# Kernel optimization log

Measured on AMD Instinct MI355X. Metric: run time of the kernel, lower is better.

## Reference

```python
import jax, jax.numpy as jnp
import numpy as np

D_MODEL = 64  # per-head dim used in the scale sqrt(d_model*2)
B, H, S, D = 4, 16, 2048, 64


def setup_inputs() -> dict:
    key = jax.random.key(0)
    kq, kk, kv, kd, ke, km = jax.random.split(key, 6)
    return {
        "Q": jax.random.normal(kq, (B, H, S, D), dtype=jnp.float32),
        "K": jax.random.normal(kk, (B, H, S, D), dtype=jnp.float32),
        "V": jax.random.normal(kv, (B, H, S, D), dtype=jnp.float32),
        "distance_matrix": jax.random.uniform(kd, (B, S, S), dtype=jnp.float32),
        "energy_matrix": jax.random.uniform(ke, (B, S, S), dtype=jnp.float32),
        "mask": jax.random.randint(km, (B, 1, S, S), 0, 2, dtype=jnp.int32),
    }


def reference(Q, K, V, distance_matrix, energy_matrix, mask):
    # distance_matrix and energy_matrix are unused by the original forward.
    scale = 1.0 / np.sqrt(D_MODEL * 2).astype(np.float32)
    scores = jnp.einsum("bhqd,bhkd->bhqk", Q, K) * scale  # [B,H,S,S]
    scores = jnp.where(mask == 0, jnp.float32(-1e9), scores)
    attn = jax.nn.softmax(scores, axis=-1)
    context = jnp.einsum("bhqk,bhkd->bhqd", attn, V)  # [B,H,S,D]
    return context
```

## Files before the change

### kernel.cpp

```cpp
#include <hip/hip_runtime.h>
#include <stdint.h>

#define DEVINL __device__ __forceinline__

typedef float f32x4 __attribute__((ext_vector_type(4)));
typedef float f32x2 __attribute__((ext_vector_type(2)));
typedef short s16x8 __attribute__((ext_vector_type(8)));
typedef short s16x4 __attribute__((ext_vector_type(4)));
typedef unsigned int u32x4 __attribute__((ext_vector_type(4)));

constexpr int Bb = 4, Hh = 16, Ss = 2048, Dd = 64;
constexpr float SCALE = 0.088388347648318447f;
constexpr float QSC = 0.088388347648318447f * 1.4426950408889634f;

DEVINL short f2bf(float x) {
  union { float f; unsigned u; } c; c.f = x;
  unsigned r = (c.u + 0x7fffu + ((c.u >> 16) & 1u)) >> 16;
  return (short)r;
}

DEVINL unsigned pkbf(float a, float b) {
  unsigned r;
  asm("v_cvt_pk_bf16_f32 %0, %1, %2" : "=v"(r) : "v"(a), "v"(b));
  return r;
}

DEVINL void gload_lds16(const short* g, short* l) {
  __builtin_amdgcn_global_load_lds(
      (const __attribute__((address_space(1))) void*)g,
      (__attribute__((address_space(3))) void*)l, 16, 0, 0);
}

__global__ void mask_to_bits(const int* __restrict__ mask,
                             unsigned long long* __restrict__ bits, int n) {
  int gid = blockIdx.x * blockDim.x + threadIdx.x;
  int stride = gridDim.x * blockDim.x;
  for (int i = gid; i < n; i += stride) {
    unsigned long long bal = __ballot(mask[i] != 0);
    if ((i & 63) == 0) bits[i >> 6] = bal;
  }
}

__global__ void kvconv(const float* __restrict__ K, const float* __restrict__ V,
                       short* __restrict__ Kimg, short* __restrict__ Vimg) {
  const int x = blockIdx.x;
  const int sel = x & 1;
  const int t = (x >> 1) & 31;
  const int bh = x >> 6;
  const int tid = threadIdx.x;
  if (sel == 0) {
    const float* Kp = K + ((size_t)bh * Ss + t * 64) * Dd;
    short* img = Kimg + ((size_t)bh * 32 + t) * 4096;
#pragma unroll
    for (int it = 0; it < 4; ++it) {
      int idx = tid + it * 256;
      int kv = idx >> 4, c = idx & 15;
      const float* kr = Kp + (size_t)kv * Dd;
      s16x4 sv;
      sv[0] = f2bf(kr[c]);
      sv[1] = f2bf(kr[c + 16]);
      sv[2] = f2bf(kr[c + 32]);
      sv[3] = f2bf(kr[c + 48]);
      *(s16x4*)(img + kv * 64 + ((4 * c) ^ ((kv & 7) << 3))) = sv;
    }
  } else {
    const float* Vp = V + ((size_t)bh * Ss + t * 64) * Dd;
    short* img = Vimg + ((size_t)bh * 32 + t) * 4096;
    const int d = tid & 63, c4 = tid >> 6;
#pragma unroll
    for (int it = 0; it < 4; ++it) {
      int c = c4 * 4 + it;
      s16x4 sv;
      sv[0] = f2bf(Vp[(size_t)(c) * Dd + d]);
      sv[1] = f2bf(Vp[(size_t)(c + 16) * Dd + d]);
      sv[2] = f2bf(Vp[(size_t)(c + 32) * Dd + d]);
      sv[3] = f2bf(Vp[(size_t)(c + 48) * Dd + d]);
      *(s16x4*)(img + d * 64 + ((4 * c) ^ ((d & 7) << 3))) = sv;
    }
  }
}

__launch_bounds__(256, 4)
__global__ void attn2(const float* __restrict__ Q,
                      const unsigned long long* __restrict__ mbits,
                      const short* __restrict__ Kimg,
                      const short* __restrict__ Vimg,
                      float* __restrict__ Out) {
  __shared__ short lds[16384];

  const int tid = threadIdx.x;
  const int lane = tid & 63;
  const int w = tid >> 6;
  const int l15 = lane & 15;
  const int lq = lane >> 4;

  const int bid = blockIdx.x;
  const int h = bid & 15;
  const int qt = (bid >> 4) & 15;
  const int b = bid >> 8;
  const int bh = b * Hh + h;

  const float* Qp = Q + (size_t)bh * Ss * Dd;
  float* Op = Out + (size_t)bh * Ss * Dd;
  const short* Kt = Kimg + (size_t)bh * 32 * 4096;
  const short* Vt = Vimg + (size_t)bh * 32 * 4096;
  const int qbW = qt * 128 + w * 32;

  s16x8 qf[2][2];
#pragma unroll
  for (int qs = 0; qs < 2; ++qs) {
    const float* qrow = Qp + (size_t)(qbW + qs * 16 + l15) * Dd;
#pragma unroll
    for (int dh = 0; dh < 2; ++dh) {
      s16x8 f;
#pragma unroll
      for (int g = 0; g < 4; ++g) {
        f32x2 v = *(const f32x2*)(qrow + 16 * g + 4 * lq + 2 * dh);
        f[g] = f2bf(v[0] * QSC);
        f[g + 4] = f2bf(v[1] * QSC);
      }
      qf[qs][dh] = f;
    }
  }

  s16x8 onesA;
  {
    short o = (l15 == 0) ? (short)0x3F80 : (short)0;
#pragma unroll
    for (int j = 0; j < 8; ++j) onesA[j] = o;
  }

  f32x4 oacc[2][4];
  f32x4 lacc[2];
#pragma unroll
  for (int qs = 0; qs < 2; ++qs) {
    lacc[qs] = f32x4{0.f, 0.f, 0.f, 0.f};
#pragma unroll
    for (int ds = 0; ds < 4; ++ds) oacc[qs][ds] = f32x4{0.f, 0.f, 0.f, 0.f};
  }

  int off[4][2];
#pragma unroll
  for (int sub = 0; sub < 4; ++sub) {
    int row = sub * 16 + l15;
    int sw = (row & 7) << 3;
    off[sub][0] = row * 64 + ((16 * lq) ^ sw);
    off[sub][1] = row * 64 + ((16 * lq + 8) ^ sw);
  }

  const unsigned long long* mbq[2];
#pragma unroll
  for (int qs = 0; qs < 2; ++qs)
    mbq[qs] = mbits + (size_t)(b * Ss + qbW + qs * 16 + l15) * 32;

  auto stage = [&](int buf, int t) {
    short* Lb = lds + buf * 8192;
    const short* gk = Kt + t * 4096 + w * 512 + lane * 8;
    const short* gv = Vt + t * 4096 + w * 512 + lane * 8;
    gload_lds16(gk, Lb + w * 512);
    gload_lds16(gk + 2048, Lb + 2048 + w * 512);
    gload_lds16(gv, Lb + 4096 + w * 512);
    gload_lds16(gv + 2048, Lb + 6144 + w * 512);
  };

  stage(0, 0);

  for (int t = 0; t < 32; ++t) {
    const int cur = t & 1;
    unsigned long long mw0 = mbq[0][t];
    unsigned long long mw1 = mbq[1][t];
    __syncthreads();
    if (t < 31) stage(cur ^ 1, t + 1);

    const short* kb = lds + cur * 8192;
    const short* vb = kb + 4096;

    f32x4 bias[2][4];
#pragma unroll
    for (int qs = 0; qs < 2; ++qs) {
      const unsigned long long mw = qs ? mw1 : mw0;
      const unsigned mlo = ~(unsigned)(mw >> (4 * lq));
      const unsigned mhi = ~(unsigned)(mw >> (32 + 4 * lq));
#pragma unroll
      for (int sub = 0; sub < 4; ++sub) {
        const unsigned wsrc = (sub < 2) ? mlo : mhi;
        const int base = 16 * (sub & 1);
#pragma unroll
        for (int r = 0; r < 4; ++r) {
          int sb = ((int)(wsrc << (31 - (base + r)))) >> 31;
          bias[qs][sub][r] = __uint_as_float((unsigned)sb & 0xCE6E6B28u);
        }
      }
    }

    f32x4 sc[2][4];
    __builtin_amdgcn_s_setprio(1);
#pragma unroll
    for (int sub = 0; sub < 4; ++sub) {
      s16x8 k0 = *(const s16x8*)(kb + off[sub][0]);
      s16x8 k1 = *(const s16x8*)(kb + off[sub][1]);
#pragma unroll
      for (int qs = 0; qs < 2; ++qs) {
        f32x4 a = bias[qs][sub];
        a = __builtin_amdgcn_mfma_f32_16x16x32_bf16(k0, qf[qs][0], a, 0, 0, 0);
        a = __builtin_amdgcn_mfma_f32_16x16x32_bf16(k1, qf[qs][1], a, 0, 0, 0);
        sc[qs][sub] = a;
      }
    }
    __builtin_amdgcn_s_setprio(0);

    s16x8 pf[2][2];
#pragma unroll
    for (int qs = 0; qs < 2; ++qs) {
#pragma unroll
      for (int sub = 0; sub < 4; ++sub) {
        f32x4 s = sc[qs][sub];
#pragma unroll
        for (int r = 0; r < 4; ++r) s[r] = __builtin_amdgcn_exp2f(s[r]);
        sc[qs][sub] = s;
      }
#pragma unroll
      for (int kvh = 0; kvh < 2; ++kvh) {
        u32x4 wv;
        wv[0] = pkbf(sc[qs][0][2 * kvh], sc[qs][1][2 * kvh]);
        wv[1] = pkbf(sc[qs][2][2 * kvh], sc[qs][3][2 * kvh]);
        wv[2] = pkbf(sc[qs][0][2 * kvh + 1], sc[qs][1][2 * kvh + 1]);
        wv[3] = pkbf(sc[qs][2][2 * kvh + 1], sc[qs][3][2 * kvh + 1]);
        pf[qs][kvh] = __builtin_bit_cast(s16x8, wv);
      }
    }

    __builtin_amdgcn_s_setprio(1);
#pragma unroll
    for (int ds = 0; ds < 4; ++ds) {
      s16x8 v0 = *(const s16x8*)(vb + off[ds][0]);
      s16x8 v1 = *(const s16x8*)(vb + off[ds][1]);
#pragma unroll
      for (int qs = 0; qs < 2; ++qs) {
        f32x4 a = oacc[qs][ds];
        a = __builtin_amdgcn_mfma_f32_16x16x32_bf16(v0, pf[qs][0], a, 0, 0, 0);
        a = __builtin_amdgcn_mfma_f32_16x16x32_bf16(v1, pf[qs][1], a, 0, 0, 0);
        oacc[qs][ds] = a;
      }
    }
#pragma unroll
    for (int qs = 0; qs < 2; ++qs) {
      lacc[qs] = __builtin_amdgcn_mfma_f32_16x16x32_bf16(onesA, pf[qs][0], lacc[qs], 0, 0, 0);
      lacc[qs] = __builtin_amdgcn_mfma_f32_16x16x32_bf16(onesA, pf[qs][1], lacc[qs], 0, 0, 0);
    }
    __builtin_amdgcn_s_setprio(0);
  }

#pragma unroll
  for (int qs = 0; qs < 2; ++qs) {
    float l = __shfl(lacc[qs][0], l15);
    float inv = 1.f / l;
    float* orow = Op + (size_t)(qbW + qs * 16 + l15) * Dd;
#pragma unroll
    for (int ds = 0; ds < 4; ++ds) {
      f32x4 v = oacc[qs][ds];
      v *= inv;
      *(f32x4*)(orow + ds * 16 + 4 * lq) = v;
    }
  }
}

template<bool USEBITS>
__launch_bounds__(256, 2)
__global__ void attn_fwd(const float* __restrict__ Q, const float* __restrict__ K,
                         const float* __restrict__ V, const int* __restrict__ mask,
                         const unsigned long long* __restrict__ mbits,
                         float* __restrict__ Out) {
  __shared__ short Ks[64 * 64];
  __shared__ short Vs[64 * 64];

  const int tid = threadIdx.x;
  const int lane = tid & 63;
  const int w = tid >> 6;
  const int l15 = lane & 15;
  const int lq = lane >> 4;

  const int bid = blockIdx.x;
  const int h = bid & 15;
  const int qt = (bid >> 4) & 7;
  const int b = bid >> 7;

  const int bh = b * Hh + h;
  const float* Qp = Q + (size_t)bh * Ss * Dd;
  const float* Kp = K + (size_t)bh * Ss * Dd;
  const float* Vp = V + (size_t)bh * Ss * Dd;
  float* Op = Out + (size_t)bh * Ss * Dd;

  const int qbW = qt * 256 + w * 64;

  s16x8 qf[4][2];
#pragma unroll
  for (int qs = 0; qs < 4; ++qs) {
    const float* qrow = Qp + (size_t)(qbW + qs * 16 + l15) * Dd;
#pragma unroll
    for (int dh = 0; dh < 2; ++dh) {
      s16x8 f;
#pragma unroll
      for (int g = 0; g < 4; ++g) {
        f32x2 v = *(const f32x2*)(qrow + 16 * g + 4 * lq + 2 * dh);
        f[g] = f2bf(v[0]);
        f[g + 4] = f2bf(v[1]);
      }
      qf[qs][dh] = f;
    }
  }

  f32x4 oacc[4][4];
  float mrun[4], lrun[4];
#pragma unroll
  for (int qs = 0; qs < 4; ++qs) {
    mrun[qs] = -1e30f;
    lrun[qs] = 0.f;
#pragma unroll
    for (int ds = 0; ds < 4; ++ds) oacc[qs][ds] = f32x4{0.f, 0.f, 0.f, 0.f};
  }

  for (int kv0 = 0; kv0 < Ss; kv0 += 64) {
    __syncthreads();
#pragma unroll
    for (int p = 0; p < 4; ++p) {
      int f = tid + p * 256;
      int kv = f >> 4;
      int c = f & 15;
      const float* krow = Kp + (size_t)(kv0 + kv) * Dd;
      s16x4 sv;
      sv[0] = f2bf(krow[c]);
      sv[1] = f2bf(krow[c + 16]);
      sv[2] = f2bf(krow[c + 32]);
      sv[3] = f2bf(krow[c + 48]);
      *(s16x4*)(Ks + kv * 64 + ((4 * c) ^ ((kv & 7) << 3))) = sv;
    }
#pragma unroll
    for (int p = 0; p < 4; ++p) {
      int f = tid + p * 256;
      int kv = f >> 4;
      int c = f & 15;
      f32x4 v = *(const f32x4*)(Vp + (size_t)(kv0 + kv) * Dd + 4 * c);
      int pv = (kv & 15) * 4 + (kv >> 4);
#pragma unroll
      for (int i = 0; i < 4; ++i) {
        int d = 4 * c + i;
        Vs[d * 64 + (pv ^ ((d & 7) << 3))] = f2bf(v[i]);
      }
    }
    __syncthreads();

    s16x8 kf[4][2];
#pragma unroll
    for (int sub = 0; sub < 4; ++sub) {
      int row = sub * 16 + l15;
      const short* base = Ks + row * 64;
      int sw = (row & 7) << 3;
      kf[sub][0] = *(const s16x8*)(base + ((16 * lq + 0) ^ sw));
      kf[sub][1] = *(const s16x8*)(base + ((16 * lq + 8) ^ sw));
    }
    s16x8 vf[4][2];
#pragma unroll
    for (int ds = 0; ds < 4; ++ds) {
      int row = ds * 16 + l15;
      const short* base = Vs + row * 64;
      int sw = (row & 7) << 3;
      vf[ds][0] = *(const s16x8*)(base + ((16 * lq + 0) ^ sw));
      vf[ds][1] = *(const s16x8*)(base + ((16 * lq + 8) ^ sw));
    }

    const int kvw = kv0 >> 6;
#pragma unroll
    for (int qs = 0; qs < 4; ++qs) {
      f32x4 sc[4];
#pragma unroll
      for (int sub = 0; sub < 4; ++sub) {
        f32x4 a = f32x4{0.f, 0.f, 0.f, 0.f};
        a = __builtin_amdgcn_mfma_f32_16x16x32_bf16(kf[sub][0], qf[qs][0], a, 0, 0, 0);
        a = __builtin_amdgcn_mfma_f32_16x16x32_bf16(kf[sub][1], qf[qs][1], a, 0, 0, 0);
        sc[sub] = a;
      }

      const int q = qbW + qs * 16 + l15;
      unsigned long long mw = 0;
      if constexpr (USEBITS) mw = mbits[(size_t)(b * Ss + q) * 32 + kvw];

      float tm = -3e38f;
#pragma unroll
      for (int sub = 0; sub < 4; ++sub) {
        f32x4 s = sc[sub];
        if constexpr (USEBITS) {
          unsigned nib = (unsigned)((mw >> (16 * sub + 4 * lq)) & 0xFULL);
#pragma unroll
          for (int r = 0; r < 4; ++r) {
            float sv = s[r] * SCALE;
            sv = ((nib >> r) & 1u) ? sv : -1e9f;
            s[r] = sv;
            tm = fmaxf(tm, sv);
          }
        } else {
          const int* mrow = mask + ((size_t)b * Ss + q) * Ss + kv0 + 16 * sub + 4 * lq;
          int4 mi = *(const int4*)mrow;
          int mv[4] = {mi.x, mi.y, mi.z, mi.w};
#pragma unroll
          for (int r = 0; r < 4; ++r) {
            float sv = s[r] * SCALE;
            sv = mv[r] ? sv : -1e9f;
            s[r] = sv;
            tm = fmaxf(tm, sv);
          }
        }
        sc[sub] = s;
      }
      tm = fmaxf(tm, __shfl_xor(tm, 16));
      tm = fmaxf(tm, __shfl_xor(tm, 32));
      float mnew = fmaxf(mrun[qs], tm);
      float corr = __expf(mrun[qs] - mnew);
      mrun[qs] = mnew;

      float ps = 0.f;
#pragma unroll
      for (int sub = 0; sub < 4; ++sub) {
        f32x4 s = sc[sub];
#pragma unroll
        for (int r = 0; r < 4; ++r) {
          float p = __expf(s[r] - mnew);
          s[r] = p;
          ps += p;
        }
        sc[sub] = s;
      }
      ps += __shfl_xor(ps, 16);
      ps += __shfl_xor(ps, 32);
      lrun[qs] = lrun[qs] * corr + ps;
#pragma unroll
      for (int ds = 0; ds < 4; ++ds) oacc[qs][ds] *= corr;

      s16x8 pf[2];
#pragma unroll
      for (int kvh = 0; kvh < 2; ++kvh) {
        s16x8 f;
#pragma unroll
        for (int j = 0; j < 8; ++j) f[j] = f2bf(sc[j & 3][2 * kvh + (j >> 2)]);
        pf[kvh] = f;
      }
#pragma unroll
      for (int ds = 0; ds < 4; ++ds) {
        f32x4 a = oacc[qs][ds];
        a = __builtin_amdgcn_mfma_f32_16x16x32_bf16(vf[ds][0], pf[0], a, 0, 0, 0);
        a = __builtin_amdgcn_mfma_f32_16x16x32_bf16(vf[ds][1], pf[1], a, 0, 0, 0);
        oacc[qs][ds] = a;
      }
    }
  }

#pragma unroll
  for (int qs = 0; qs < 4; ++qs) {
    float inv = 1.f / lrun[qs];
    float* orow = Op + (size_t)(qbW + qs * 16 + l15) * Dd;
#pragma unroll
    for (int ds = 0; ds < 4; ++ds) {
      f32x4 v = oacc[qs][ds];
      v *= inv;
      *(f32x4*)(orow + ds * 16 + 4 * lq) = v;
    }
  }
}

extern "C" void kernel_launch(void* const* d_in, const int* in_sizes, int n_in,
                              void* d_out, int out_size, void* d_ws, size_t ws_size,
                              hipStream_t stream) {
  const float* Q = (const float*)d_in[0];
  const float* K = (const float*)d_in[1];
  const float* V = (const float*)d_in[2];
  const int* mask = (const int*)d_in[5];
  float* out = (float*)d_out;

  const int nmask = Bb * Ss * Ss;
  const size_t bitsB = (size_t)(nmask / 64) * 8;
  const size_t imgB = (size_t)Bb * Hh * 32 * 4096 * 2;
  const size_t need = bitsB + 2 * imgB;

  if (d_ws && ws_size >= need) {
    unsigned long long* bits = (unsigned long long*)d_ws;
    short* Kimg = (short*)((char*)d_ws + bitsB);
    short* Vimg = (short*)((char*)d_ws + bitsB + imgB);
    mask_to_bits<<<2048, 256, 0, stream>>>(mask, bits, nmask);
    kvconv<<<Bb * Hh * 32 * 2, 256, 0, stream>>>(K, V, Kimg, Vimg);
    attn2<<<Bb * Hh * (Ss / 128), 256, 0, stream>>>(Q, bits, Kimg, Vimg, out);
  } else if (d_ws && ws_size >= bitsB) {
    unsigned long long* bits = (unsigned long long*)d_ws;
    mask_to_bits<<<2048, 256, 0, stream>>>(mask, bits, nmask);
    attn_fwd<true><<<Bb * Hh * (Ss / 256), 256, 0, stream>>>(Q, K, V, mask, bits, out);
  } else {
    attn_fwd<false><<<Bb * Hh * (Ss / 256), 256, 0, stream>>>(Q, K, V, mask, nullptr, out);
  }
}
```

Baseline: 134.4 us.

## Halve per-wave query tile, double grid, and remap blocks for XCD locality

Each wave now handles 16 query rows instead of 32, so a block covers 64 queries and the grid doubles to 2048 blocks. Launch bounds rise to 5 blocks per SM to exploit the lower register use. Block indices are remapped with an 8-way interleave so blocks sharing the same batch-head land on the same XCD, improving L2 reuse of the K/V images. The trade-off is that each K/V tile loaded into LDS is reused by half as many query rows, doubling K/V staging traffic and the number of barriers per unit of work.

```diff
diff --git a/kernel.cpp b/kernel.cpp
--- a/kernel.cpp
+++ b/kernel.cpp
@@ -80,7 +80,7 @@
   }
 }
 
-__launch_bounds__(256, 4)
+__launch_bounds__(256, 5)
 __global__ void attn2(const float* __restrict__ Q,
                       const unsigned long long* __restrict__ mbits,
                       const short* __restrict__ Kimg,
@@ -94,22 +94,20 @@
   const int l15 = lane & 15;
   const int lq = lane >> 4;
 
-  const int bid = blockIdx.x;
-  const int h = bid & 15;
-  const int qt = (bid >> 4) & 15;
-  const int b = bid >> 8;
-  const int bh = b * Hh + h;
+  const int nb = ((blockIdx.x & 7) << 8) | (blockIdx.x >> 3);
+  const int qt = nb & 31;
+  const int bh = nb >> 5;
+  const int b = bh >> 4;
 
   const float* Qp = Q + (size_t)bh * Ss * Dd;
   float* Op = Out + (size_t)bh * Ss * Dd;
   const short* Kt = Kimg + (size_t)bh * 32 * 4096;
   const short* Vt = Vimg + (size_t)bh * 32 * 4096;
-  const int qbW = qt * 128 + w * 32;
-
-  s16x8 qf[2][2];
-#pragma unroll
-  for (int qs = 0; qs < 2; ++qs) {
-    const float* qrow = Qp + (size_t)(qbW + qs * 16 + l15) * Dd;
+  const int qbW = qt * 64 + w * 16;
+
+  s16x8 qf[2];
+  {
+    const float* qrow = Qp + (size_t)(qbW + l15) * Dd;
 #pragma unroll
     for (int dh = 0; dh < 2; ++dh) {
       s16x8 f;
@@ -119,7 +117,7 @@
         f[g] = f2bf(v[0] * QSC);
         f[g + 4] = f2bf(v[1] * QSC);
       }
-      qf[qs][dh] = f;
+      qf[dh] = f;
     }
   }
 
@@ -130,14 +128,10 @@
     for (int j = 0; j < 8; ++j) onesA[j] = o;
   }
 
-  f32x4 oacc[2][4];
-  f32x4 lacc[2];
-#pragma unroll
-  for (int qs = 0; qs < 2; ++qs) {
-    lacc[qs] = f32x4{0.f, 0.f, 0.f, 0.f};
-#pragma unroll
-    for (int ds = 0; ds < 4; ++ds) oacc[qs][ds] = f32x4{0.f, 0.f, 0.f, 0.f};
-  }
+  f32x4 oacc[4];
+  f32x4 lacc = f32x4{0.f, 0.f, 0.f, 0.f};
+#pragma unroll
+  for (int ds = 0; ds < 4; ++ds) oacc[ds] = f32x4{0.f, 0.f, 0.f, 0.f};
 
   int off[4][2];
 #pragma unroll
@@ -148,10 +142,7 @@
     off[sub][1] = row * 64 + ((16 * lq + 8) ^ sw);
   }
 
-  const unsigned long long* mbq[2];
-#pragma unroll
-  for (int qs = 0; qs < 2; ++qs)
-    mbq[qs] = mbits + (size_t)(b * Ss + qbW + qs * 16 + l15) * 32;
+  const unsigned long long* mbq = mbits + (size_t)(b * Ss + qbW + l15) * 32;
 
   auto stage = [&](int buf, int t) {
     short* Lb = lds + buf * 8192;
@@ -167,18 +158,15 @@
 
   for (int t = 0; t < 32; ++t) {
     const int cur = t & 1;
-    unsigned long long mw0 = mbq[0][t];
-    unsigned long long mw1 = mbq[1][t];
+    unsigned long long mw = mbq[t];
     __syncthreads();
     if (t < 31) stage(cur ^ 1, t + 1);
 
     const short* kb = lds + cur * 8192;
     const short* vb = kb + 4096;
 
-    f32x4 bias[2][4];
-#pragma unroll
-    for (int qs = 0; qs < 2; ++qs) {
-      const unsigned long long mw = qs ? mw1 : mw0;
+    f32x4 bias[4];
+    {
       const unsigned mlo = ~(unsigned)(mw >> (4 * lq));
       const unsigned mhi = ~(unsigned)(mw >> (32 + 4 * lq));
 #pragma unroll
@@ -188,46 +176,40 @@
 #pragma unroll
         for (int r = 0; r < 4; ++r) {
           int sb = ((int)(wsrc << (31 - (base + r)))) >> 31;
-          bias[qs][sub][r] = __uint_as_float((unsigned)sb & 0xCE6E6B28u);
+          bias[sub][r] = __uint_as_float((unsigned)sb & 0xCE6E6B28u);
         }
       }
     }
 
-    f32x4 sc[2][4];
+    f32x4 sc[4];
     __builtin_amdgcn_s_setprio(1);
 #pragma unroll
     for (int sub = 0; sub < 4; ++sub) {
       s16x8 k0 = *(const s16x8*)(kb + off[sub][0]);
       s16x8 k1 = *(const s16x8*)(kb + off[sub][1]);
-#pragma unroll
-      for (int qs = 0; qs < 2; ++qs) {
-        f32x4 a = bias[qs][sub];
-        a = __builtin_amdgcn_mfma_f32_16x16x32_bf16(k0, qf[qs][0], a, 0, 0, 0);
-        a = __builtin_amdgcn_mfma_f32_16x16x32_bf16(k1, qf[qs][1], a, 0, 0, 0);
-        sc[qs][sub] = a;
-      }
+      f32x4 a = bias[sub];
+      a = __builtin_amdgcn_mfma_f32_16x16x32_bf16(k0, qf[0], a, 0, 0, 0);
+      a = __builtin_amdgcn_mfma_f32_16x16x32_bf16(k1, qf[1], a, 0, 0, 0);
+      sc[sub] = a;
     }
     __builtin_amdgcn_s_setprio(0);
 
-    s16x8 pf[2][2];
-#pragma unroll
-    for (int qs = 0; qs < 2; ++qs) {
-#pragma unroll
-      for (int sub = 0; sub < 4; ++sub) {
-        f32x4 s = sc[qs][sub];
-#pragma unroll
-        for (int r = 0; r < 4; ++r) s[r] = __builtin_amdgcn_exp2f(s[r]);
-        sc[qs][sub] = s;
-      }
-#pragma unroll
-      for (int kvh = 0; kvh < 2; ++kvh) {
-        u32x4 wv;
-        wv[0] = pkbf(sc[qs][0][2 * kvh], sc[qs][1][2 * kvh]);
-        wv[1] = pkbf(sc[qs][2][2 * kvh], sc[qs][3][2 * kvh]);
-        wv[2] = pkbf(sc[qs][0][2 * kvh + 1], sc[qs][1][2 * kvh + 1]);
-        wv[3] = pkbf(sc[qs][2][2 * kvh + 1], sc[qs][3][2 * kvh + 1]);
-        pf[qs][kvh] = __builtin_bit_cast(s16x8, wv);
-      }
+    s16x8 pf[2];
+#pragma unroll
+    for (int sub = 0; sub < 4; ++sub) {
+      f32x4 s = sc[sub];
+#pragma unroll
+      for (int r = 0; r < 4; ++r) s[r] = __builtin_amdgcn_exp2f(s[r]);
+      sc[sub] = s;
+    }
+#pragma unroll
+    for (int kvh = 0; kvh < 2; ++kvh) {
+      u32x4 wv;
+      wv[0] = pkbf(sc[0][2 * kvh], sc[1][2 * kvh]);
+      wv[1] = pkbf(sc[2][2 * kvh], sc[3][2 * kvh]);
+      wv[2] = pkbf(sc[0][2 * kvh + 1], sc[1][2 * kvh + 1]);
+      wv[3] = pkbf(sc[2][2 * kvh + 1], sc[3][2 * kvh + 1]);
+      pf[kvh] = __builtin_bit_cast(s16x8, wv);
     }
 
     __builtin_amdgcn_s_setprio(1);
@@ -235,30 +217,23 @@
     for (int ds = 0; ds < 4; ++ds) {
       s16x8 v0 = *(const s16x8*)(vb + off[ds][0]);
       s16x8 v1 = *(const s16x8*)(vb + off[ds][1]);
-#pragma unroll
-      for (int qs = 0; qs < 2; ++qs) {
-        f32x4 a = oacc[qs][ds];
-        a = __builtin_amdgcn_mfma_f32_16x16x32_bf16(v0, pf[qs][0], a, 0, 0, 0);
-        a = __builtin_amdgcn_mfma_f32_16x16x32_bf16(v1, pf[qs][1], a, 0, 0, 0);
-        oacc[qs][ds] = a;
-      }
-    }
-#pragma unroll
-    for (int qs = 0; qs < 2; ++qs) {
-      lacc[qs] = __builtin_amdgcn_mfma_f32_16x16x32_bf16(onesA, pf[qs][0], lacc[qs], 0, 0, 0);
-      lacc[qs] = __builtin_amdgcn_mfma_f32_16x16x32_bf16(onesA, pf[qs][1], lacc[qs], 0, 0, 0);
-    }
+      f32x4 a = oacc[ds];
+      a = __builtin_amdgcn_mfma_f32_16x16x32_bf16(v0, pf[0], a, 0, 0, 0);
+      a = __builtin_amdgcn_mfma_f32_16x16x32_bf16(v1, pf[1], a, 0, 0, 0);
+      oacc[ds] = a;
+    }
+    lacc = __builtin_amdgcn_mfma_f32_16x16x32_bf16(onesA, pf[0], lacc, 0, 0, 0);
+    lacc = __builtin_amdgcn_mfma_f32_16x16x32_bf16(onesA, pf[1], lacc, 0, 0, 0);
     __builtin_amdgcn_s_setprio(0);
   }
 
-#pragma unroll
-  for (int qs = 0; qs < 2; ++qs) {
-    float l = __shfl(lacc[qs][0], l15);
+  {
+    float l = __shfl(lacc[0], l15);
     float inv = 1.f / l;
-    float* orow = Op + (size_t)(qbW + qs * 16 + l15) * Dd;
+    float* orow = Op + (size_t)(qbW + l15) * Dd;
 #pragma unroll
     for (int ds = 0; ds < 4; ++ds) {
-      f32x4 v = oacc[qs][ds];
+      f32x4 v = oacc[ds];
       v *= inv;
       *(f32x4*)(orow + ds * 16 + 4 * lq) = v;
     }
@@ -487,7 +462,7 @@
     short* Vimg = (short*)((char*)d_ws + bitsB + imgB);
     mask_to_bits<<<2048, 256, 0, stream>>>(mask, bits, nmask);
     kvconv<<<Bb * Hh * 32 * 2, 256, 0, stream>>>(K, V, Kimg, Vimg);
-    attn2<<<Bb * Hh * (Ss / 128), 256, 0, stream>>>(Q, bits, Kimg, Vimg, out);
+    attn2<<<Bb * Hh * (Ss / 64), 256, 0, stream>>>(Q, bits, Kimg, Vimg, out);
   } else if (d_ws && ws_size >= bitsB) {
     unsigned long long* bits = (unsigned long long*)d_ws;
     mask_to_bits<<<2048, 256, 0, stream>>>(mask, bits, nmask);
```

Result: slower. 144.0 us (+7.1%).

## Fuse prep kernels and load K/V fragments directly to registers

Applied to the files above, without the earlier changes.

Merges the mask bit-packing and K/V bf16 conversion into one prep launch, and lays the K/V images out in MFMA fragment order so the attention kernel can load them straight from global memory into registers with no LDS or barriers. Each wave now handles 64 queries instead of 32 (256 per block, 512 blocks), and block indices are swizzled so that blocks sharing a head are grouped. K/V fragments for the next tile are prefetched into registers after each matmul phase. The intent is to remove LDS staging, barrier synchronisation and one launch. In exchange, register pressure and occupancy change, and loads go through L2 without explicit sharing between waves.

```diff
diff --git a/kernel.cpp b/kernel.cpp
--- a/kernel.cpp
+++ b/kernel.cpp
@@ -25,10 +25,212 @@
   return r;
 }
 
-DEVINL void gload_lds16(const short* g, short* l) {
-  __builtin_amdgcn_global_load_lds(
-      (const __attribute__((address_space(1))) void*)g,
-      (__attribute__((address_space(3))) void*)l, 16, 0, 0);
+__global__ void prep(const float* __restrict__ K, const float* __restrict__ V,
+                     const int* __restrict__ mask,
+                     short* __restrict__ Kimg, short* __restrict__ Vimg,
+                     unsigned long long* __restrict__ bits) {
+  const int x = blockIdx.x;
+  const int tid = threadIdx.x;
+  if (x < 4096) {
+    const int sel = x & 1;
+    const int t = (x >> 1) & 31;
+    const int bh = x >> 6;
+    short* img = (sel ? Vimg : Kimg) + ((size_t)bh * 32 + t) * 4096;
+    const float* src = (sel ? V : K) + (size_t)bh * Ss * Dd;
+#pragma unroll
+    for (int p = 0; p < 2; ++p) {
+      const int pr = tid + p * 256;
+      const int f = pr >> 6;
+      const int lane = pr & 63;
+      const int l15 = lane & 15, lq = lane >> 4;
+      const int P = 16 * lq + 8 * (f & 1);
+      const int fs = f >> 1;
+      s16x8 o;
+      if (sel == 0) {
+        const float* kr = src + (size_t)(t * 64 + fs * 16 + l15) * Dd + (P >> 2);
+#pragma unroll
+        for (int jj = 0; jj < 2; ++jj)
+#pragma unroll
+          for (int m = 0; m < 4; ++m)
+            o[jj * 4 + m] = f2bf(kr[jj + 16 * m]);
+      } else {
+        const float* vc = src + (size_t)(t * 64 + (P >> 2)) * Dd + fs * 16 + l15;
+#pragma unroll
+        for (int jj = 0; jj < 2; ++jj)
+#pragma unroll
+          for (int m = 0; m < 4; ++m)
+            o[jj * 4 + m] = f2bf(vc[(size_t)(jj + 16 * m) * Dd]);
+      }
+      *(s16x8*)(img + pr * 8) = o;
+    }
+  } else {
+    const int gid = (x - 4096) * 256 + tid;
+    const int stride = 1024 * 256;
+    const int n = Bb * Ss * Ss;
+    for (int i = gid; i < n; i += stride) {
+      unsigned long long bal = __ballot(mask[i] != 0);
+      if ((i & 63) == 0) bits[i >> 6] = bal;
+    }
+  }
+}
+
+__launch_bounds__(256, 2)
+__global__ void attn3(const float* __restrict__ Q,
+                      const unsigned long long* __restrict__ mbits,
+                      const short* __restrict__ Kimg,
+                      const short* __restrict__ Vimg,
+                      float* __restrict__ Out) {
+  const int tid = threadIdx.x;
+  const int lane = tid & 63;
+  const int w = tid >> 6;
+  const int l15 = lane & 15;
+  const int lq = lane >> 4;
+
+  const int nb = ((blockIdx.x & 7) << 6) | (blockIdx.x >> 3);
+  const int qt = nb & 7;
+  const int bh = nb >> 3;
+  const int b = bh >> 4;
+
+  const float* Qp = Q + (size_t)bh * Ss * Dd;
+  float* Op = Out + (size_t)bh * Ss * Dd;
+  const short* Kt = Kimg + (size_t)bh * 32 * 4096 + lane * 8;
+  const short* Vt = Vimg + (size_t)bh * 32 * 4096 + lane * 8;
+  const int qbW = qt * 256 + w * 64;
+
+  s16x8 qf[4][2];
+#pragma unroll
+  for (int qs = 0; qs < 4; ++qs) {
+    const float* qrow = Qp + (size_t)(qbW + qs * 16 + l15) * Dd;
+#pragma unroll
+    for (int dh = 0; dh < 2; ++dh) {
+      s16x8 f;
+#pragma unroll
+      for (int g = 0; g < 4; ++g) {
+        f32x2 v = *(const f32x2*)(qrow + 16 * g + 4 * lq + 2 * dh);
+        f[g] = f2bf(v[0] * QSC);
+        f[g + 4] = f2bf(v[1] * QSC);
+      }
+      qf[qs][dh] = f;
+    }
+  }
+
+  s16x8 onesA;
+  {
+    short o = (l15 == 0) ? (short)0x3F80 : (short)0;
+#pragma unroll
+    for (int j = 0; j < 8; ++j) onesA[j] = o;
+  }
+
+  f32x4 oacc[4][4];
+  f32x4 lacc[4];
+#pragma unroll
+  for (int qs = 0; qs < 4; ++qs) {
+    lacc[qs] = f32x4{0.f, 0.f, 0.f, 0.f};
+#pragma unroll
+    for (int ds = 0; ds < 4; ++ds) oacc[qs][ds] = f32x4{0.f, 0.f, 0.f, 0.f};
+  }
+
+  const unsigned long long* mbq = mbits + (size_t)(b * Ss + qbW + l15) * 32;
+
+  s16x8 kf[8], vf[8];
+#pragma unroll
+  for (int f = 0; f < 8; ++f) kf[f] = *(const s16x8*)(Kt + f * 512);
+#pragma unroll
+  for (int f = 0; f < 8; ++f) vf[f] = *(const s16x8*)(Vt + f * 512);
+
+  for (int t = 0; t < 32; ++t) {
+    unsigned long long mw[4];
+#pragma unroll
+    for (int qs = 0; qs < 4; ++qs) mw[qs] = mbq[qs * 512 + t];
+
+    f32x4 sc[4][4];
+#pragma unroll
+    for (int qs = 0; qs < 4; ++qs) {
+      const unsigned mlo = ~(unsigned)(mw[qs] >> (4 * lq));
+      const unsigned mhi = ~(unsigned)(mw[qs] >> (32 + 4 * lq));
+#pragma unroll
+      for (int sub = 0; sub < 4; ++sub) {
+        const unsigned wsrc = (sub < 2) ? mlo : mhi;
+        const int base = 16 * (sub & 1);
+#pragma unroll
+        for (int r = 0; r < 4; ++r) {
+          int sb = ((int)(wsrc << (31 - (base + r)))) >> 31;
+          sc[qs][sub][r] = __uint_as_float((unsigned)sb & 0xCE6E6B28u);
+        }
+      }
+    }
+
+    __builtin_amdgcn_s_setprio(1);
+#pragma unroll
+    for (int sub = 0; sub < 4; ++sub)
+#pragma unroll
+      for (int qs = 0; qs < 4; ++qs) {
+        sc[qs][sub] = __builtin_amdgcn_mfma_f32_16x16x32_bf16(kf[sub * 2], qf[qs][0], sc[qs][sub], 0, 0, 0);
+        sc[qs][sub] = __builtin_amdgcn_mfma_f32_16x16x32_bf16(kf[sub * 2 + 1], qf[qs][1], sc[qs][sub], 0, 0, 0);
+      }
+    __builtin_amdgcn_s_setprio(0);
+
+    if (t < 31) {
+      const short* nk = Kt + (t + 1) * 4096;
+#pragma unroll
+      for (int f = 0; f < 8; ++f) kf[f] = *(const s16x8*)(nk + f * 512);
+    }
+
+    s16x8 pf[4][2];
+#pragma unroll
+    for (int qs = 0; qs < 4; ++qs) {
+#pragma unroll
+      for (int sub = 0; sub < 4; ++sub) {
+        f32x4 s = sc[qs][sub];
+#pragma unroll
+        for (int r = 0; r < 4; ++r) s[r] = __builtin_amdgcn_exp2f(s[r]);
+        sc[qs][sub] = s;
+      }
+#pragma unroll
+      for (int kvh = 0; kvh < 2; ++kvh) {
+        u32x4 wv;
+        wv[0] = pkbf(sc[qs][0][2 * kvh], sc[qs][1][2 * kvh]);
+        wv[1] = pkbf(sc[qs][2][2 * kvh], sc[qs][3][2 * kvh]);
+        wv[2] = pkbf(sc[qs][0][2 * kvh + 1], sc[qs][1][2 * kvh + 1]);
+        wv[3] = pkbf(sc[qs][2][2 * kvh + 1], sc[qs][3][2 * kvh + 1]);
+        pf[qs][kvh] = __builtin_bit_cast(s16x8, wv);
+      }
+    }
+
+    __builtin_amdgcn_s_setprio(1);
+#pragma unroll
+    for (int ds = 0; ds < 4; ++ds)
+#pragma unroll
+      for (int qs = 0; qs < 4; ++qs) {
+        oacc[qs][ds] = __builtin_amdgcn_mfma_f32_16x16x32_bf16(vf[ds * 2], pf[qs][0], oacc[qs][ds], 0, 0, 0);
+        oacc[qs][ds] = __builtin_amdgcn_mfma_f32_16x16x32_bf16(vf[ds * 2 + 1], pf[qs][1], oacc[qs][ds], 0, 0, 0);
+      }
+#pragma unroll
+    for (int qs = 0; qs < 4; ++qs) {
+      lacc[qs] = __builtin_amdgcn_mfma_f32_16x16x32_bf16(onesA, pf[qs][0], lacc[qs], 0, 0, 0);
+      lacc[qs] = __builtin_amdgcn_mfma_f32_16x16x32_bf16(onesA, pf[qs][1], lacc[qs], 0, 0, 0);
+    }
+    __builtin_amdgcn_s_setprio(0);
+
+    if (t < 31) {
+      const short* nv = Vt + (t + 1) * 4096;
+#pragma unroll
+      for (int f = 0; f < 8; ++f) vf[f] = *(const s16x8*)(nv + f * 512);
+    }
+  }
+
+#pragma unroll
+  for (int qs = 0; qs < 4; ++qs) {
+    float l = __shfl(lacc[qs][0], l15);
+    float inv = 1.f / l;
+    float* orow = Op + (size_t)(qbW + qs * 16 + l15) * Dd;
+#pragma unroll
+    for (int ds = 0; ds < 4; ++ds) {
+      f32x4 v = oacc[qs][ds];
+      v *= inv;
+      *(f32x4*)(orow + ds * 16 + 4 * lq) = v;
+    }
+  }
 }
 
 __global__ void mask_to_bits(const int* __restrict__ mask,
@@ -38,230 +240,6 @@
   for (int i = gid; i < n; i += stride) {
     unsigned long long bal = __ballot(mask[i] != 0);
     if ((i & 63) == 0) bits[i >> 6] = bal;
-  }
-}
-
-__global__ void kvconv(const float* __restrict__ K, const float* __restrict__ V,
-                       short* __restrict__ Kimg, short* __restrict__ Vimg) {
-  const int x = blockIdx.x;
-  const int sel = x & 1;
-  const int t = (x >> 1) & 31;
-  const int bh = x >> 6;
-  const int tid = threadIdx.x;
-  if (sel == 0) {
-    const float* Kp = K + ((size_t)bh * Ss + t * 64) * Dd;
-    short* img = Kimg + ((size_t)bh * 32 + t) * 4096;
-#pragma unroll
-    for (int it = 0; it < 4; ++it) {
-      int idx = tid + it * 256;
-      int kv = idx >> 4, c = idx & 15;
-      const float* kr = Kp + (size_t)kv * Dd;
-      s16x4 sv;
-      sv[0] = f2bf(kr[c]);
-      sv[1] = f2bf(kr[c + 16]);
-      sv[2] = f2bf(kr[c + 32]);
-      sv[3] = f2bf(kr[c + 48]);
-      *(s16x4*)(img + kv * 64 + ((4 * c) ^ ((kv & 7) << 3))) = sv;
-    }
-  } else {
-    const float* Vp = V + ((size_t)bh * Ss + t * 64) * Dd;
-    short* img = Vimg + ((size_t)bh * 32 + t) * 4096;
-    const int d = tid & 63, c4 = tid >> 6;
-#pragma unroll
-    for (int it = 0; it < 4; ++it) {
-      int c = c4 * 4 + it;
-      s16x4 sv;
-      sv[0] = f2bf(Vp[(size_t)(c) * Dd + d]);
-      sv[1] = f2bf(Vp[(size_t)(c + 16) * Dd + d]);
-      sv[2] = f2bf(Vp[(size_t)(c + 32) * Dd + d]);
-      sv[3] = f2bf(Vp[(size_t)(c + 48) * Dd + d]);
-      *(s16x4*)(img + d * 64 + ((4 * c) ^ ((d & 7) << 3))) = sv;
-    }
-  }
-}
-
-__launch_bounds__(256, 4)
-__global__ void attn2(const float* __restrict__ Q,
-                      const unsigned long long* __restrict__ mbits,
-                      const short* __restrict__ Kimg,
-                      const short* __restrict__ Vimg,
-                      float* __restrict__ Out) {
-  __shared__ short lds[16384];
-
-  const int tid = threadIdx.x;
-  const int lane = tid & 63;
-  const int w = tid >> 6;
-  const int l15 = lane & 15;
-  const int lq = lane >> 4;
-
-  const int bid = blockIdx.x;
-  const int h = bid & 15;
-  const int qt = (bid >> 4) & 15;
-  const int b = bid >> 8;
-  const int bh = b * Hh + h;
-
-  const float* Qp = Q + (size_t)bh * Ss * Dd;
-  float* Op = Out + (size_t)bh * Ss * Dd;
-  const short* Kt = Kimg + (size_t)bh * 32 * 4096;
-  const short* Vt = Vimg + (size_t)bh * 32 * 4096;
-  const int qbW = qt * 128 + w * 32;
-
-  s16x8 qf[2][2];
-#pragma unroll
-  for (int qs = 0; qs < 2; ++qs) {
-    const float* qrow = Qp + (size_t)(qbW + qs * 16 + l15) * Dd;
-#pragma unroll
-    for (int dh = 0; dh < 2; ++dh) {
-      s16x8 f;
-#pragma unroll
-      for (int g = 0; g < 4; ++g) {
-        f32x2 v = *(const f32x2*)(qrow + 16 * g + 4 * lq + 2 * dh);
-        f[g] = f2bf(v[0] * QSC);
-        f[g + 4] = f2bf(v[1] * QSC);
-      }
-      qf[qs][dh] = f;
-    }
-  }
-
-  s16x8 onesA;
-  {
-    short o = (l15 == 0) ? (short)0x3F80 : (short)0;
-#pragma unroll
-    for (int j = 0; j < 8; ++j) onesA[j] = o;
-  }
-
-  f32x4 oacc[2][4];
-  f32x4 lacc[2];
-#pragma unroll
-  for (int qs = 0; qs < 2; ++qs) {
-    lacc[qs] = f32x4{0.f, 0.f, 0.f, 0.f};
-#pragma unroll
-    for (int ds = 0; ds < 4; ++ds) oacc[qs][ds] = f32x4{0.f, 0.f, 0.f, 0.f};
-  }
-
-  int off[4][2];
-#pragma unroll
-  for (int sub = 0; sub < 4; ++sub) {
-    int row = sub * 16 + l15;
-    int sw = (row & 7) << 3;
-    off[sub][0] = row * 64 + ((16 * lq) ^ sw);
-    off[sub][1] = row * 64 + ((16 * lq + 8) ^ sw);
-  }
-
-  const unsigned long long* mbq[2];
-#pragma unroll
-  for (int qs = 0; qs < 2; ++qs)
-    mbq[qs] = mbits + (size_t)(b * Ss + qbW + qs * 16 + l15) * 32;
-
-  auto stage = [&](int buf, int t) {
-    short* Lb = lds + buf * 8192;
-    const short* gk = Kt + t * 4096 + w * 512 + lane * 8;
-    const short* gv = Vt + t * 4096 + w * 512 + lane * 8;
-    gload_lds16(gk, Lb + w * 512);
-    gload_lds16(gk + 2048, Lb + 2048 + w * 512);
-    gload_lds16(gv, Lb + 4096 + w * 512);
-    gload_lds16(gv + 2048, Lb + 6144 + w * 512);
-  };
-
-  stage(0, 0);
-
-  for (int t = 0; t < 32; ++t) {
-    const int cur = t & 1;
-    unsigned long long mw0 = mbq[0][t];
-    unsigned long long mw1 = mbq[1][t];
-    __syncthreads();
-    if (t < 31) stage(cur ^ 1, t + 1);
-
-    const short* kb = lds + cur * 8192;
-    const short* vb = kb + 4096;
-
-    f32x4 bias[2][4];
-#pragma unroll
-    for (int qs = 0; qs < 2; ++qs) {
-      const unsigned long long mw = qs ? mw1 : mw0;
-      const unsigned mlo = ~(unsigned)(mw >> (4 * lq));
-      const unsigned mhi = ~(unsigned)(mw >> (32 + 4 * lq));
-#pragma unroll
-      for (int sub = 0; sub < 4; ++sub) {
-        const unsigned wsrc = (sub < 2) ? mlo : mhi;
-        const int base = 16 * (sub & 1);
-#pragma unroll
-        for (int r = 0; r < 4; ++r) {
-          int sb = ((int)(wsrc << (31 - (base + r)))) >> 31;
-          bias[qs][sub][r] = __uint_as_float((unsigned)sb & 0xCE6E6B28u);
-        }
-      }
-    }
-
-    f32x4 sc[2][4];
-    __builtin_amdgcn_s_setprio(1);
-#pragma unroll
-    for (int sub = 0; sub < 4; ++sub) {
-      s16x8 k0 = *(const s16x8*)(kb + off[sub][0]);
-      s16x8 k1 = *(const s16x8*)(kb + off[sub][1]);
-#pragma unroll
-      for (int qs = 0; qs < 2; ++qs) {
-        f32x4 a = bias[qs][sub];
-        a = __builtin_amdgcn_mfma_f32_16x16x32_bf16(k0, qf[qs][0], a, 0, 0, 0);
-        a = __builtin_amdgcn_mfma_f32_16x16x32_bf16(k1, qf[qs][1], a, 0, 0, 0);
-        sc[qs][sub] = a;
-      }
-    }
-    __builtin_amdgcn_s_setprio(0);
-
-    s16x8 pf[2][2];
-#pragma unroll
-    for (int qs = 0; qs < 2; ++qs) {
-#pragma unroll
-      for (int sub = 0; sub < 4; ++sub) {
-        f32x4 s = sc[qs][sub];
-#pragma unroll
-        for (int r = 0; r < 4; ++r) s[r] = __builtin_amdgcn_exp2f(s[r]);
-        sc[qs][sub] = s;
-      }
-#pragma unroll
-      for (int kvh = 0; kvh < 2; ++kvh) {
-        u32x4 wv;
-        wv[0] = pkbf(sc[qs][0][2 * kvh], sc[qs][1][2 * kvh]);
-        wv[1] = pkbf(sc[qs][2][2 * kvh], sc[qs][3][2 * kvh]);
-        wv[2] = pkbf(sc[qs][0][2 * kvh + 1], sc[qs][1][2 * kvh + 1]);
-        wv[3] = pkbf(sc[qs][2][2 * kvh + 1], sc[qs][3][2 * kvh + 1]);
-        pf[qs][kvh] = __builtin_bit_cast(s16x8, wv);
-      }
-    }
-
-    __builtin_amdgcn_s_setprio(1);
-#pragma unroll
-    for (int ds = 0; ds < 4; ++ds) {
-      s16x8 v0 = *(const s16x8*)(vb + off[ds][0]);
-      s16x8 v1 = *(const s16x8*)(vb + off[ds][1]);
-#pragma unroll
-      for (int qs = 0; qs < 2; ++qs) {
-        f32x4 a = oacc[qs][ds];
-        a = __builtin_amdgcn_mfma_f32_16x16x32_bf16(v0, pf[qs][0], a, 0, 0, 0);
-        a = __builtin_amdgcn_mfma_f32_16x16x32_bf16(v1, pf[qs][1], a, 0, 0, 0);
-        oacc[qs][ds] = a;
-      }
-    }
-#pragma unroll
-    for (int qs = 0; qs < 2; ++qs) {
-      lacc[qs] = __builtin_amdgcn_mfma_f32_16x16x32_bf16(onesA, pf[qs][0], lacc[qs], 0, 0, 0);
-      lacc[qs] = __builtin_amdgcn_mfma_f32_16x16x32_bf16(onesA, pf[qs][1], lacc[qs], 0, 0, 0);
-    }
-    __builtin_amdgcn_s_setprio(0);
-  }
-
-#pragma unroll
-  for (int qs = 0; qs < 2; ++qs) {
-    float l = __shfl(lacc[qs][0], l15);
-    float inv = 1.f / l;
-    float* orow = Op + (size_t)(qbW + qs * 16 + l15) * Dd;
-#pragma unroll
-    for (int ds = 0; ds < 4; ++ds) {
-      f32x4 v = oacc[qs][ds];
-      v *= inv;
-      *(f32x4*)(orow + ds * 16 + 4 * lq) = v;
-    }
   }
 }
 
@@ -485,9 +463,8 @@
     unsigned long long* bits = (unsigned long long*)d_ws;
     short* Kimg = (short*)((char*)d_ws + bitsB);
     short* Vimg = (short*)((char*)d_ws + bitsB + imgB);
-    mask_to_bits<<<2048, 256, 0, stream>>>(mask, bits, nmask);
-    kvconv<<<Bb * Hh * 32 * 2, 256, 0, stream>>>(K, V, Kimg, Vimg);
-    attn2<<<Bb * Hh * (Ss / 128), 256, 0, stream>>>(Q, bits, Kimg, Vimg, out);
+    prep<<<5120, 256, 0, stream>>>(K, V, mask, Kimg, Vimg, bits);
+    attn3<<<512, 256, 0, stream>>>(Q, bits, Kimg, Vimg, out);
   } else if (d_ws && ws_size >= bitsB) {
     unsigned long long* bits = (unsigned long long*)d_ws;
     mask_to_bits<<<2048, 256, 0, stream>>>(mask, bits, nmask);
```

After: 160.6 us. 19.5% more time.

## Merge mask packing and KV conversion into one kernel; interleave exp with MFMA

Applied to the files above, without the earlier changes.

Combines the mask-to-bitmask and K/V bf16 conversion kernels into a single prep launch, with blocks split by index. This removes one kernel launch and lets the two memory-bound jobs run at the same time. In the attention loop it splits the two query sub-tiles and interleaves the exp2 of one sub-tile with the MFMAs of the other, so transcendental work overlaps matrix-core work. This adds register pressure and depends on the compiler keeping the intended order.

```diff
diff --git a/kernel.cpp b/kernel.cpp
--- a/kernel.cpp
+++ b/kernel.cpp
@@ -31,51 +31,53 @@
       (__attribute__((address_space(3))) void*)l, 16, 0, 0);
 }
 
-__global__ void mask_to_bits(const int* __restrict__ mask,
-                             unsigned long long* __restrict__ bits, int n) {
-  int gid = blockIdx.x * blockDim.x + threadIdx.x;
-  int stride = gridDim.x * blockDim.x;
-  for (int i = gid; i < n; i += stride) {
-    unsigned long long bal = __ballot(mask[i] != 0);
-    if ((i & 63) == 0) bits[i >> 6] = bal;
-  }
-}
-
-__global__ void kvconv(const float* __restrict__ K, const float* __restrict__ V,
-                       short* __restrict__ Kimg, short* __restrict__ Vimg) {
+__global__ void prep(const float* __restrict__ K, const float* __restrict__ V,
+                     const int* __restrict__ mask,
+                     short* __restrict__ Kimg, short* __restrict__ Vimg,
+                     unsigned long long* __restrict__ bits) {
   const int x = blockIdx.x;
-  const int sel = x & 1;
-  const int t = (x >> 1) & 31;
-  const int bh = x >> 6;
   const int tid = threadIdx.x;
-  if (sel == 0) {
-    const float* Kp = K + ((size_t)bh * Ss + t * 64) * Dd;
-    short* img = Kimg + ((size_t)bh * 32 + t) * 4096;
-#pragma unroll
-    for (int it = 0; it < 4; ++it) {
-      int idx = tid + it * 256;
-      int kv = idx >> 4, c = idx & 15;
-      const float* kr = Kp + (size_t)kv * Dd;
-      s16x4 sv;
-      sv[0] = f2bf(kr[c]);
-      sv[1] = f2bf(kr[c + 16]);
-      sv[2] = f2bf(kr[c + 32]);
-      sv[3] = f2bf(kr[c + 48]);
-      *(s16x4*)(img + kv * 64 + ((4 * c) ^ ((kv & 7) << 3))) = sv;
+  if (x < 4096) {
+    const int sel = x & 1;
+    const int t = (x >> 1) & 31;
+    const int bh = x >> 6;
+    if (sel == 0) {
+      const float* Kp = K + ((size_t)bh * Ss + t * 64) * Dd;
+      short* img = Kimg + ((size_t)bh * 32 + t) * 4096;
+#pragma unroll
+      for (int it = 0; it < 4; ++it) {
+        int idx = tid + it * 256;
+        int kv = idx >> 4, c = idx & 15;
+        const float* kr = Kp + (size_t)kv * Dd;
+        s16x4 sv;
+        sv[0] = f2bf(kr[c]);
+        sv[1] = f2bf(kr[c + 16]);
+        sv[2] = f2bf(kr[c + 32]);
+        sv[3] = f2bf(kr[c + 48]);
+        *(s16x4*)(img + kv * 64 + ((4 * c) ^ ((kv & 7) << 3))) = sv;
+      }
+    } else {
+      const float* Vp = V + ((size_t)bh * Ss + t * 64) * Dd;
+      short* img = Vimg + ((size_t)bh * 32 + t) * 4096;
+      const int d = tid & 63, c4 = tid >> 6;
+#pragma unroll
+      for (int it = 0; it < 4; ++it) {
+        int c = c4 * 4 + it;
+        s16x4 sv;
+        sv[0] = f2bf(Vp[(size_t)(c) * Dd + d]);
+        sv[1] = f2bf(Vp[(size_t)(c + 16) * Dd + d]);
+        sv[2] = f2bf(Vp[(size_t)(c + 32) * Dd + d]);
+        sv[3] = f2bf(Vp[(size_t)(c + 48) * Dd + d]);
+        *(s16x4*)(img + d * 64 + ((4 * c) ^ ((d & 7) << 3))) = sv;
+      }
     }
   } else {
-    const float* Vp = V + ((size_t)bh * Ss + t * 64) * Dd;
-    short* img = Vimg + ((size_t)bh * 32 + t) * 4096;
-    const int d = tid & 63, c4 = tid >> 6;
-#pragma unroll
-    for (int it = 0; it < 4; ++it) {
-      int c = c4 * 4 + it;
-      s16x4 sv;
-      sv[0] = f2bf(Vp[(size_t)(c) * Dd + d]);
-      sv[1] = f2bf(Vp[(size_t)(c + 16) * Dd + d]);
-      sv[2] = f2bf(Vp[(size_t)(c + 32) * Dd + d]);
-      sv[3] = f2bf(Vp[(size_t)(c + 48) * Dd + d]);
-      *(s16x4*)(img + d * 64 + ((4 * c) ^ ((d & 7) << 3))) = sv;
+    const int gid = (x - 4096) * 256 + tid;
+    const int stride = 1024 * 256;
+    const int n = Bb * Ss * Ss;
+    for (int i = gid; i < n; i += stride) {
+      unsigned long long bal = __ballot(mask[i] != 0);
+      if ((i & 63) == 0) bits[i >> 6] = bal;
     }
   }
 }
@@ -175,79 +177,100 @@
     const short* kb = lds + cur * 8192;
     const short* vb = kb + 4096;
 
-    f32x4 bias[2][4];
-#pragma unroll
-    for (int qs = 0; qs < 2; ++qs) {
-      const unsigned long long mw = qs ? mw1 : mw0;
-      const unsigned mlo = ~(unsigned)(mw >> (4 * lq));
-      const unsigned mhi = ~(unsigned)(mw >> (32 + 4 * lq));
+    f32x4 bias0[4], bias1[4];
+    {
+      const unsigned mlo0 = ~(unsigned)(mw0 >> (4 * lq));
+      const unsigned mhi0 = ~(unsigned)(mw0 >> (32 + 4 * lq));
+      const unsigned mlo1 = ~(unsigned)(mw1 >> (4 * lq));
+      const unsigned mhi1 = ~(unsigned)(mw1 >> (32 + 4 * lq));
 #pragma unroll
       for (int sub = 0; sub < 4; ++sub) {
-        const unsigned wsrc = (sub < 2) ? mlo : mhi;
+        const unsigned w0 = (sub < 2) ? mlo0 : mhi0;
+        const unsigned w1 = (sub < 2) ? mlo1 : mhi1;
         const int base = 16 * (sub & 1);
 #pragma unroll
         for (int r = 0; r < 4; ++r) {
-          int sb = ((int)(wsrc << (31 - (base + r)))) >> 31;
-          bias[qs][sub][r] = __uint_as_float((unsigned)sb & 0xCE6E6B28u);
+          int s0 = ((int)(w0 << (31 - (base + r)))) >> 31;
+          int s1 = ((int)(w1 << (31 - (base + r)))) >> 31;
+          bias0[sub][r] = __uint_as_float((unsigned)s0 & 0xCE6E6B28u);
+          bias1[sub][r] = __uint_as_float((unsigned)s1 & 0xCE6E6B28u);
         }
       }
     }
 
-    f32x4 sc[2][4];
+    f32x4 sc0[4], sc1[4];
     __builtin_amdgcn_s_setprio(1);
 #pragma unroll
     for (int sub = 0; sub < 4; ++sub) {
       s16x8 k0 = *(const s16x8*)(kb + off[sub][0]);
       s16x8 k1 = *(const s16x8*)(kb + off[sub][1]);
-#pragma unroll
-      for (int qs = 0; qs < 2; ++qs) {
-        f32x4 a = bias[qs][sub];
-        a = __builtin_amdgcn_mfma_f32_16x16x32_bf16(k0, qf[qs][0], a, 0, 0, 0);
-        a = __builtin_amdgcn_mfma_f32_16x16x32_bf16(k1, qf[qs][1], a, 0, 0, 0);
-        sc[qs][sub] = a;
+      f32x4 a0 = __builtin_amdgcn_mfma_f32_16x16x32_bf16(k0, qf[0][0], bias0[sub], 0, 0, 0);
+      sc0[sub] = __builtin_amdgcn_mfma_f32_16x16x32_bf16(k1, qf[0][1], a0, 0, 0, 0);
+      f32x4 a1 = __builtin_amdgcn_mfma_f32_16x16x32_bf16(k0, qf[1][0], bias1[sub], 0, 0, 0);
+      sc1[sub] = __builtin_amdgcn_mfma_f32_16x16x32_bf16(k1, qf[1][1], a1, 0, 0, 0);
+      if (sub > 0) {
+        f32x4 s = sc0[sub - 1];
+#pragma unroll
+        for (int r = 0; r < 4; ++r) s[r] = __builtin_amdgcn_exp2f(s[r]);
+        sc0[sub - 1] = s;
       }
     }
     __builtin_amdgcn_s_setprio(0);
-
-    s16x8 pf[2][2];
-#pragma unroll
-    for (int qs = 0; qs < 2; ++qs) {
-#pragma unroll
-      for (int sub = 0; sub < 4; ++sub) {
-        f32x4 s = sc[qs][sub];
-#pragma unroll
-        for (int r = 0; r < 4; ++r) s[r] = __builtin_amdgcn_exp2f(s[r]);
-        sc[qs][sub] = s;
-      }
-#pragma unroll
-      for (int kvh = 0; kvh < 2; ++kvh) {
-        u32x4 wv;
-        wv[0] = pkbf(sc[qs][0][2 * kvh], sc[qs][1][2 * kvh]);
-        wv[1] = pkbf(sc[qs][2][2 * kvh], sc[qs][3][2 * kvh]);
-        wv[2] = pkbf(sc[qs][0][2 * kvh + 1], sc[qs][1][2 * kvh + 1]);
-        wv[3] = pkbf(sc[qs][2][2 * kvh + 1], sc[qs][3][2 * kvh + 1]);
-        pf[qs][kvh] = __builtin_bit_cast(s16x8, wv);
-      }
-    }
-
+    {
+      f32x4 s = sc0[3];
+#pragma unroll
+      for (int r = 0; r < 4; ++r) s[r] = __builtin_amdgcn_exp2f(s[r]);
+      sc0[3] = s;
+    }
+
+    s16x8 pf0[2];
+#pragma unroll
+    for (int kvh = 0; kvh < 2; ++kvh) {
+      u32x4 wv;
+      wv[0] = pkbf(sc0[0][2 * kvh], sc0[1][2 * kvh]);
+      wv[1] = pkbf(sc0[2][2 * kvh], sc0[3][2 * kvh]);
+      wv[2] = pkbf(sc0[0][2 * kvh + 1], sc0[1][2 * kvh + 1]);
+      wv[3] = pkbf(sc0[2][2 * kvh + 1], sc0[3][2 * kvh + 1]);
+      pf0[kvh] = __builtin_bit_cast(s16x8, wv);
+    }
     __builtin_amdgcn_s_setprio(1);
 #pragma unroll
     for (int ds = 0; ds < 4; ++ds) {
       s16x8 v0 = *(const s16x8*)(vb + off[ds][0]);
       s16x8 v1 = *(const s16x8*)(vb + off[ds][1]);
-#pragma unroll
-      for (int qs = 0; qs < 2; ++qs) {
-        f32x4 a = oacc[qs][ds];
-        a = __builtin_amdgcn_mfma_f32_16x16x32_bf16(v0, pf[qs][0], a, 0, 0, 0);
-        a = __builtin_amdgcn_mfma_f32_16x16x32_bf16(v1, pf[qs][1], a, 0, 0, 0);
-        oacc[qs][ds] = a;
-      }
-    }
-#pragma unroll
-    for (int qs = 0; qs < 2; ++qs) {
-      lacc[qs] = __builtin_amdgcn_mfma_f32_16x16x32_bf16(onesA, pf[qs][0], lacc[qs], 0, 0, 0);
-      lacc[qs] = __builtin_amdgcn_mfma_f32_16x16x32_bf16(onesA, pf[qs][1], lacc[qs], 0, 0, 0);
-    }
+      f32x4 a = oacc[0][ds];
+      a = __builtin_amdgcn_mfma_f32_16x16x32_bf16(v0, pf0[0], a, 0, 0, 0);
+      oacc[0][ds] = __builtin_amdgcn_mfma_f32_16x16x32_bf16(v1, pf0[1], a, 0, 0, 0);
+      f32x4 s = sc1[ds];
+#pragma unroll
+      for (int r = 0; r < 4; ++r) s[r] = __builtin_amdgcn_exp2f(s[r]);
+      sc1[ds] = s;
+    }
+    lacc[0] = __builtin_amdgcn_mfma_f32_16x16x32_bf16(onesA, pf0[0], lacc[0], 0, 0, 0);
+    lacc[0] = __builtin_amdgcn_mfma_f32_16x16x32_bf16(onesA, pf0[1], lacc[0], 0, 0, 0);
+    __builtin_amdgcn_s_setprio(0);
+
+    s16x8 pf1[2];
+#pragma unroll
+    for (int kvh = 0; kvh < 2; ++kvh) {
+      u32x4 wv;
+      wv[0] = pkbf(sc1[0][2 * kvh], sc1[1][2 * kvh]);
+      wv[1] = pkbf(sc1[2][2 * kvh], sc1[3][2 * kvh]);
+      wv[2] = pkbf(sc1[0][2 * kvh + 1], sc1[1][2 * kvh + 1]);
+      wv[3] = pkbf(sc1[2][2 * kvh + 1], sc1[3][2 * kvh + 1]);
+      pf1[kvh] = __builtin_bit_cast(s16x8, wv);
+    }
+    __builtin_amdgcn_s_setprio(1);
+#pragma unroll
+    for (int ds = 0; ds < 4; ++ds) {
+      s16x8 v0 = *(const s16x8*)(vb + off[ds][0]);
+      s16x8 v1 = *(const s16x8*)(vb + off[ds][1]);
+      f32x4 a = oacc[1][ds];
+      a = __builtin_amdgcn_mfma_f32_16x16x32_bf16(v0, pf1[0], a, 0, 0, 0);
+      oacc[1][ds] = __builtin_amdgcn_mfma_f32_16x16x32_bf16(v1, pf1[1], a, 0, 0, 0);
+    }
+    lacc[1] = __builtin_amdgcn_mfma_f32_16x16x32_bf16(onesA, pf1[0], lacc[1], 0, 0, 0);
+    lacc[1] = __builtin_amdgcn_mfma_f32_16x16x32_bf16(onesA, pf1[1], lacc[1], 0, 0, 0);
     __builtin_amdgcn_s_setprio(0);
   }
 
@@ -262,6 +285,16 @@
       v *= inv;
       *(f32x4*)(orow + ds * 16 + 4 * lq) = v;
     }
+  }
+}
+
+__global__ void mask_to_bits(const int* __restrict__ mask,
+                             unsigned long long* __restrict__ bits, int n) {
+  int gid = blockIdx.x * blockDim.x + threadIdx.x;
+  int stride = gridDim.x * blockDim.x;
+  for (int i = gid; i < n; i += stride) {
+    unsigned long long bal = __ballot(mask[i] != 0);
+    if ((i & 63) == 0) bits[i >> 6] = bal;
   }
 }
 
@@ -485,8 +518,7 @@
     unsigned long long* bits = (unsigned long long*)d_ws;
     short* Kimg = (short*)((char*)d_ws + bitsB);
     short* Vimg = (short*)((char*)d_ws + bitsB + imgB);
-    mask_to_bits<<<2048, 256, 0, stream>>>(mask, bits, nmask);
-    kvconv<<<Bb * Hh * 32 * 2, 256, 0, stream>>>(K, V, Kimg, Vimg);
+    prep<<<5120, 256, 0, stream>>>(K, V, mask, Kimg, Vimg, bits);
     attn2<<<Bb * Hh * (Ss / 128), 256, 0, stream>>>(Q, bits, Kimg, Vimg, out);
   } else if (d_ws && ws_size >= bitsB) {
     unsigned long long* bits = (unsigned long long*)d_ws;
```

Result: slower. 139.8 us (+4.1%).
